# Optimization experiments

Hardware: AMD Instinct MI355X
Metric: run time of the kernel (lower is better)

The kernel has to match this reference:

```python
import jax, jax.numpy as jnp
import numpy as np

HEAD_SIZE = 64
INPUT_SIZE = 1024
B, T = 4, 4096


def setup_inputs() -> dict:
    key = jax.random.key(0)
    ks = jax.random.split(key, 7)
    s = 1.0 / np.sqrt(INPUT_SIZE)
    return {
        "x": jax.random.normal(ks[0], (B, T, INPUT_SIZE), dtype=jnp.float32),
        "Wk": jax.random.uniform(ks[1], (INPUT_SIZE, HEAD_SIZE), jnp.float32, -s, s),
        "bk": jax.random.uniform(ks[2], (HEAD_SIZE,), jnp.float32, -s, s),
        "Wq": jax.random.uniform(ks[3], (INPUT_SIZE, HEAD_SIZE), jnp.float32, -s, s),
        "bq": jax.random.uniform(ks[4], (HEAD_SIZE,), jnp.float32, -s, s),
        "Wv": jax.random.uniform(ks[5], (INPUT_SIZE, HEAD_SIZE), jnp.float32, -s, s),
        "bv": jax.random.uniform(ks[6], (HEAD_SIZE,), jnp.float32, -s, s),
    }


def reference(x, Wk, bk, Wq, bq, Wv, bv) -> jnp.ndarray:
    # x: [B, T, D]
    Tlen = x.shape[1]
    k = x @ Wk + bk          # [B, T, H]
    q = x @ Wq + bq          # [B, T, H]
    v = x @ Wv + bv          # [B, T, H]
    scale = 1.0 / jnp.sqrt(jnp.float32(HEAD_SIZE))
    # NOTE: original computes k @ q^T (not q @ k^T) -- keep that exact math.
    w = jnp.einsum("bth,bsh->bts", k, q) * scale  # [B, T, T]
    causal = jnp.tril(jnp.ones((Tlen, Tlen), dtype=bool))
    w = jnp.where(causal, w, -jnp.inf)
    w = jax.nn.softmax(w, axis=-1)
    out = jnp.einsum("bts,bsh->bth", w, v)        # [B, T, H]
    return out
```

## Files before the change

### kernel.cpp

```cpp
#include <hip/hip_runtime.h>
#include <hip/hip_bf16.h>
#include <stdint.h>

typedef __attribute__((ext_vector_type(8))) short short8;
typedef __attribute__((ext_vector_type(4))) float floatx4;

#define HD 64
#define D_IN 1024
#define TLEN 4096
#define NB 4
#define PPB 144
#define LDP 72
#define SL2E 0.18033688011112042f

__device__ __forceinline__ short f2bf(float f) {
    union { float f; uint32_t u; } v{f};
    uint32_t u = v.u;
    uint32_t r = (u + 0x7FFFu + ((u >> 16) & 1u)) >> 16;
    return (short)r;
}

__device__ __forceinline__ float bf2f(short s) {
    union { uint32_t u; float f; } v;
    v.u = ((uint32_t)(uint16_t)s) << 16;
    return v.f;
}

__device__ __forceinline__ uint32_t pk2(float a, float b) {
    __hip_bfloat162 h = __float22bfloat162_rn(float2{a, b});
    union { __hip_bfloat162 h; uint32_t u; } c{h};
    return c.u;
}

__device__ __forceinline__ void ld_lds16(const void* g, void* l) {
    __builtin_amdgcn_global_load_lds(
        (const __attribute__((address_space(1))) uint32_t*)g,
        (__attribute__((address_space(3))) uint32_t*)l, 16, 0, 0);
}

__global__ __launch_bounds__(256) void prep_w(const float* __restrict__ Wk,
                                              const float* __restrict__ Wq,
                                              const float* __restrict__ Wv,
                                              short* __restrict__ wt) {
    int i = blockIdx.x * 256 + threadIdx.x;
    int j  = i & 7;
    int l  = (i >> 3) & 63;
    int ks = (i >> 9) & 1;
    int rest = i >> 10;
    int f  = rest % 12;
    int kt = rest / 12;
    int mat = f >> 2, nt = f & 3;
    int n = nt * 16 + (l & 15);
    int k = kt * 64 + ks * 32 + (l >> 4) * 8 + j;
    const float* W = (mat == 0) ? Wk : ((mat == 1) ? Wq : Wv);
    wt[i] = f2bf(W[(size_t)k * 64 + n]);
}

__global__ __launch_bounds__(256) void proj(const float* __restrict__ x,
                                            const float* __restrict__ bk,
                                            const float* __restrict__ bq,
                                            const float* __restrict__ bv,
                                            const short* __restrict__ wt,
                                            short* __restrict__ ko,
                                            short* __restrict__ qo,
                                            short* __restrict__ vt) {
    __shared__ float xs[2][2048];
    __shared__ short ws2[2][12288];

    int tid = threadIdx.x;
    int wave = tid >> 6, lane = tid & 63;
    int quad = lane >> 4, l16 = lane & 15;
    int row0 = blockIdx.x * 32;
    int wbase = tid & ~63;

    floatx4 acc[2][3];
#pragma unroll
    for (int mt = 0; mt < 2; mt++)
#pragma unroll
        for (int fi = 0; fi < 3; fi++) acc[mt][fi] = (floatx4){0.f, 0.f, 0.f, 0.f};

    auto stage = [&](int kt, int buf) {
#pragma unroll
        for (int it = 0; it < 2; it++) {
            int s = it * 256 + tid;
            int r = s >> 4, p = s & 15;
            int c = (((p >> 1) ^ (r & 7)) << 1) | (p & 1);
            ld_lds16(x + (size_t)(row0 + r) * D_IN + kt * 64 + c * 4,
                     &xs[buf][(it * 256 + wbase) * 4]);
        }
#pragma unroll
        for (int it = 0; it < 6; it++) {
            int s = it * 256 + tid;
            ld_lds16(wt + (size_t)kt * 12288 + (size_t)s * 8,
                     &ws2[buf][(it * 256 + wbase) * 8]);
        }
    };

    stage(0, 0);
    for (int kt = 0; kt < 16; kt++) {
        int buf = kt & 1;
        __syncthreads();
        if (kt < 15) stage(kt + 1, buf ^ 1);
#pragma unroll
        for (int ks = 0; ks < 2; ks++) {
            short8 av[2];
#pragma unroll
            for (int mt = 0; mt < 2; mt++) {
                int r = mt * 16 + l16;
                int g = ks * 4 + quad;
                const float4* pp = reinterpret_cast<const float4*>(
                    &xs[buf][r * 64 + ((g ^ (r & 7)) << 1) * 4]);
                float4 f0 = pp[0], f1 = pp[1];
                union { uint32_t u[4]; short8 s; } cv;
                cv.u[0] = pk2(f0.x, f0.y); cv.u[1] = pk2(f0.z, f0.w);
                cv.u[2] = pk2(f1.x, f1.y); cv.u[3] = pk2(f1.z, f1.w);
                av[mt] = cv.s;
            }
#pragma unroll
            for (int fi = 0; fi < 3; fi++) {
                int f = wave * 3 + fi;
                short8 bf = *reinterpret_cast<const short8*>(
                    &ws2[buf][((f * 2 + ks) * 64 + lane) * 8]);
#pragma unroll
                for (int mt = 0; mt < 2; mt++)
                    acc[mt][fi] = __builtin_amdgcn_mfma_f32_16x16x32_bf16(av[mt], bf, acc[mt][fi], 0, 0, 0);
            }
        }
    }

#pragma unroll
    for (int fi = 0; fi < 3; fi++) {
        int f = wave * 3 + fi;
        int mat = f >> 2, nt = f & 3;
        int col = nt * 16 + l16;
        const float* bias = (mat == 0) ? bk : ((mat == 1) ? bq : bv);
        float bb = bias[col];
#pragma unroll
        for (int mt = 0; mt < 2; mt++)
#pragma unroll
            for (int reg = 0; reg < 4; reg++) {
                float v = acc[mt][fi][reg] + bb;
                int row = row0 + mt * 16 + quad * 4 + reg;
                if (mat == 0) ko[(size_t)row * HD + col] = f2bf(v * SL2E);
                else if (mat == 1) qo[(size_t)row * HD + col] = f2bf(v);
                else {
                    int bt = row >> 12, tl = row & 4095;
                    vt[(size_t)bt * HD * TLEN + (size_t)col * TLEN + tl] = f2bf(v);
                }
            }
    }
}

template<int SPLIT>
__global__ __launch_bounds__(256) void attn_kern(const short* __restrict__ kb,
                                                 const short* __restrict__ qb,
                                                 const short* __restrict__ vtw,
                                                 short* __restrict__ pO,
                                                 float* __restrict__ pL,
                                                 float* __restrict__ out) {
    __shared__ short Ks[2][4096];
    __shared__ short Vs[2][4096];
    __shared__ short Ps[128 * LDP];

    int tid = threadIdx.x;
    int wave = tid >> 6, lane = tid & 63;
    int quad = lane >> 4, l16 = lane & 15;
    int wbase = tid & ~63;
    int batch = blockIdx.y;

    int tile, j0, j1, slot = 0, nparts = 1;
    if (SPLIT) {
        int bx = blockIdx.x;
        int t = 0, accb = 0;
        for (;;) { int p = (2 * t + 9) >> 3; if (bx < accb + p) break; accb += p; ++t; }
        tile = t;
        j0 = (bx - accb) * 8;
        int je = j0 + 8, lim = 2 * tile + 2;
        j1 = je < lim ? je : lim;
        slot = batch * PPB + bx;
        nparts = (2 * tile + 9) >> 3;
    } else {
        tile = 31 - blockIdx.x;
        j0 = 0; j1 = 2 * tile + 2;
    }
    int t0 = tile * 128;
    int jd = 2 * tile;
    size_t base = (size_t)batch * TLEN * HD;
    const short* vbase = vtw + (size_t)batch * HD * TLEN;

    short8 kf[2][2];
#pragma unroll
    for (int mt = 0; mt < 2; mt++) {
        int trow = t0 + wave * 32 + mt * 16 + l16;
#pragma unroll
        for (int ks = 0; ks < 2; ks++)
            kf[mt][ks] = *reinterpret_cast<const short8*>(kb + base + (size_t)trow * HD + ks * 32 + quad * 8);
    }

    floatx4 o_acc[2][4];
#pragma unroll
    for (int mt = 0; mt < 2; mt++)
#pragma unroll
        for (int ht = 0; ht < 4; ht++) o_acc[mt][ht] = (floatx4){0.f, 0.f, 0.f, 0.f};
    float l_p[2] = {0.f, 0.f};

    auto stage = [&](int j, int buf) {
        int s0 = j * 64;
#pragma unroll
        for (int it = 0; it < 2; it++) {
            int s = it * 256 + tid;
            int r = s >> 3, c = (s & 7) ^ (r & 7);
            ld_lds16(qb + base + (size_t)(s0 + r) * HD + c * 8,
                     &Ks[buf][(it * 256 + wbase) * 8]);
            ld_lds16(vbase + (size_t)r * TLEN + s0 + c * 8,
                     &Vs[buf][(it * 256 + wbase) * 8]);
        }
    };

    stage(j0, 0);
    for (int j = j0; j < j1; ++j) {
        int buf = (j - j0) & 1;
        __syncthreads();
        if (j + 1 < j1) stage(j + 1, buf ^ 1);

        if (j == jd + 1 && wave < 2) continue;

        floatx4 sacc[2][4];
#pragma unroll
        for (int mt = 0; mt < 2; mt++)
#pragma unroll
            for (int nt = 0; nt < 4; nt++) sacc[mt][nt] = (floatx4){0.f, 0.f, 0.f, 0.f};
#pragma unroll
        for (int ks = 0; ks < 2; ks++)
#pragma unroll
            for (int nt = 0; nt < 4; nt++) {
                int r = nt * 16 + l16, g = ks * 4 + quad;
                short8 a = *reinterpret_cast<const short8*>(
                    &Ks[buf][r * 64 + (g ^ (r & 7)) * 8]);
#pragma unroll
                for (int mt = 0; mt < 2; mt++)
                    sacc[mt][nt] = __builtin_amdgcn_mfma_f32_16x16x32_bf16(a, kf[mt][ks], sacc[mt][nt], 0, 0, 0);
            }

        float pv[2][4][4];
#pragma unroll
        for (int mt = 0; mt < 2; mt++)
#pragma unroll
            for (int nt = 0; nt < 4; nt++)
#pragma unroll
                for (int reg = 0; reg < 4; reg++)
                    pv[mt][nt][reg] = __builtin_amdgcn_exp2f(sacc[mt][nt][reg]);
        if (j >= jd) {
            int s0 = j * 64;
#pragma unroll
            for (int mt = 0; mt < 2; mt++) {
                int t_g = t0 + wave * 32 + mt * 16 + l16;
#pragma unroll
                for (int nt = 0; nt < 4; nt++) {
                    int s_g = s0 + nt * 16 + quad * 4;
#pragma unroll
                    for (int reg = 0; reg < 4; reg++)
                        if (s_g + reg > t_g) pv[mt][nt][reg] = 0.f;
                }
            }
        }
#pragma unroll
        for (int mt = 0; mt < 2; mt++) {
            l_p[mt] += ((pv[mt][0][0] + pv[mt][0][1]) + (pv[mt][0][2] + pv[mt][0][3]))
                     + ((pv[mt][1][0] + pv[mt][1][1]) + (pv[mt][1][2] + pv[mt][1][3]))
                     + ((pv[mt][2][0] + pv[mt][2][1]) + (pv[mt][2][2] + pv[mt][2][3]))
                     + ((pv[mt][3][0] + pv[mt][3][1]) + (pv[mt][3][2] + pv[mt][3][3]));
#pragma unroll
            for (int nt = 0; nt < 4; nt++) {
                union { uint32_t u[2]; uint64_t q; } w;
                w.u[0] = pk2(pv[mt][nt][0], pv[mt][nt][1]);
                w.u[1] = pk2(pv[mt][nt][2], pv[mt][nt][3]);
                int row = wave * 32 + mt * 16 + l16;
                *reinterpret_cast<uint64_t*>(&Ps[row * LDP + nt * 16 + quad * 4]) = w.q;
            }
        }

#pragma unroll
        for (int ks = 0; ks < 2; ks++) {
            short8 a[2];
#pragma unroll
            for (int mt = 0; mt < 2; mt++)
                a[mt] = *reinterpret_cast<const short8*>(
                    &Ps[(wave * 32 + mt * 16 + l16) * LDP + ks * 32 + quad * 8]);
#pragma unroll
            for (int ht = 0; ht < 4; ht++) {
                int r = ht * 16 + l16, g = ks * 4 + quad;
                short8 b = *reinterpret_cast<const short8*>(
                    &Vs[buf][r * 64 + (g ^ (r & 7)) * 8]);
#pragma unroll
                for (int mt = 0; mt < 2; mt++)
                    o_acc[mt][ht] = __builtin_amdgcn_mfma_f32_16x16x32_bf16(a[mt], b, o_acc[mt][ht], 0, 0, 0);
            }
        }
    }

#pragma unroll
    for (int mt = 0; mt < 2; mt++) {
        l_p[mt] += __shfl_xor(l_p[mt], 16);
        l_p[mt] += __shfl_xor(l_p[mt], 32);
    }

    if (SPLIT && nparts > 1) {
        short* po = pO + (size_t)slot * 8192;
#pragma unroll
        for (int mt = 0; mt < 2; mt++)
#pragma unroll
            for (int ht = 0; ht < 4; ht++)
#pragma unroll
                for (int reg = 0; reg < 4; reg++) {
                    int lr = wave * 32 + mt * 16 + quad * 4 + reg;
                    po[lr * 64 + ht * 16 + l16] = f2bf(o_acc[mt][ht][reg]);
                }
        if (quad == 0) {
#pragma unroll
            for (int mt = 0; mt < 2; mt++)
                pL[(size_t)slot * 128 + wave * 32 + mt * 16 + l16] = l_p[mt];
        }
    } else {
#pragma unroll
        for (int mt = 0; mt < 2; mt++) {
#pragma unroll
            for (int reg = 0; reg < 4; reg++) {
                float L = __shfl(l_p[mt], quad * 4 + reg, 64);
                float inv = 1.0f / L;
                int t = t0 + wave * 32 + mt * 16 + quad * 4 + reg;
#pragma unroll
                for (int ht = 0; ht < 4; ht++)
                    out[base + (size_t)t * HD + ht * 16 + l16] = o_acc[mt][ht][reg] * inv;
            }
        }
    }
}

__global__ __launch_bounds__(256) void attn_combine(const short* __restrict__ pO,
                                                    const float* __restrict__ pL,
                                                    float* __restrict__ out) {
    int tile = blockIdx.x + 4, batch = blockIdx.y;
    int nparts = (2 * tile + 9) >> 3;
    int a = tile >> 2, r = tile & 3;
    int slot0 = batch * PPB + 2 * a * (a + 1) + r * (a + 1);
    int t = threadIdx.x;
    int off = t * 32;
    int row = off >> 6;
    int col0 = off & 63;

    float L = 0.f;
    float acc[32];
#pragma unroll
    for (int i = 0; i < 32; i++) acc[i] = 0.f;

    for (int p = 0; p < nparts; ++p) {
        int slot = slot0 + p;
        L += pL[(size_t)slot * 128 + row];
        const short* src = pO + (size_t)slot * 8192 + off;
#pragma unroll
        for (int c = 0; c < 4; c++) {
            short8 v = *reinterpret_cast<const short8*>(src + c * 8);
#pragma unroll
            for (int i = 0; i < 8; i++) acc[c * 8 + i] += bf2f(v[i]);
        }
    }
    float inv = 1.0f / L;
    float4* dstp = reinterpret_cast<float4*>(out + (size_t)batch * TLEN * HD +
                                             (size_t)(tile * 128 + row) * HD + col0);
#pragma unroll
    for (int c = 0; c < 8; c++) {
        float4 v;
        v.x = acc[c * 4 + 0] * inv; v.y = acc[c * 4 + 1] * inv;
        v.z = acc[c * 4 + 2] * inv; v.w = acc[c * 4 + 3] * inv;
        dstp[c] = v;
    }
}

extern "C" void kernel_launch(void* const* d_in, const int* in_sizes, int n_in,
                              void* d_out, int out_size, void* d_ws, size_t ws_size,
                              hipStream_t stream) {
    const float* x  = (const float*)d_in[0];
    const float* Wk = (const float*)d_in[1];
    const float* bk = (const float*)d_in[2];
    const float* Wq = (const float*)d_in[3];
    const float* bq = (const float*)d_in[4];
    const float* Wv = (const float*)d_in[5];
    const float* bv = (const float*)d_in[6];
    float* out = (float*)d_out;

    const size_t nrow = (size_t)NB * TLEN;
    short* ko = (short*)d_ws;
    short* qo = ko + nrow * HD;
    short* vt = qo + nrow * HD;
    short* wt = vt + nrow * HD;
    short* pO = wt + 3 * 64 * 1024;
    float* pL = (float*)(pO + (size_t)NB * PPB * 8192);
    size_t need = (size_t)((char*)(pL + (size_t)NB * PPB * 128) - (char*)d_ws);

    prep_w<<<768, 256, 0, stream>>>(Wk, Wq, Wv, wt);
    proj<<<512, 256, 0, stream>>>(x, bk, bq, bv, wt, ko, qo, vt);
    if (ws_size >= need) {
        attn_kern<1><<<dim3(PPB, NB), 256, 0, stream>>>(ko, qo, vt, pO, pL, out);
        attn_combine<<<dim3(28, NB), 256, 0, stream>>>(pO, pL, out);
    } else {
        attn_kern<0><<<dim3(32, NB), 256, 0, stream>>>(ko, qo, vt, nullptr, nullptr, out);
    }
}
```

Measured before the change: 152.5 us.

## Split-K projection with two wave groups and 64-row tiles reduced through LDS

```diff
diff --git a/kernel.cpp b/kernel.cpp
--- a/kernel.cpp
+++ b/kernel.cpp
@@ -12,6 +12,7 @@
 #define PPB 144
 #define LDP 72
 #define SL2E 0.18033688011112042f
+#define WSZ 196608
 
 __device__ __forceinline__ short f2bf(float f) {
     union { float f; uint32_t u; } v{f};
@@ -45,18 +46,17 @@
     int i = blockIdx.x * 256 + threadIdx.x;
     int j  = i & 7;
     int l  = (i >> 3) & 63;
-    int ks = (i >> 9) & 1;
-    int rest = i >> 10;
+    int rest = i >> 9;
     int f  = rest % 12;
-    int kt = rest / 12;
+    int ck = rest / 12;
     int mat = f >> 2, nt = f & 3;
     int n = nt * 16 + (l & 15);
-    int k = kt * 64 + ks * 32 + (l >> 4) * 8 + j;
+    int k = ck * 32 + (l >> 4) * 8 + j;
     const float* W = (mat == 0) ? Wk : ((mat == 1) ? Wq : Wv);
     wt[i] = f2bf(W[(size_t)k * 64 + n]);
 }
 
-__global__ __launch_bounds__(256) void proj(const float* __restrict__ x,
+__global__ __launch_bounds__(512) void proj(const float* __restrict__ x,
                                             const float* __restrict__ bk,
                                             const float* __restrict__ bq,
                                             const float* __restrict__ bv,
@@ -64,90 +64,104 @@
                                             short* __restrict__ ko,
                                             short* __restrict__ qo,
                                             short* __restrict__ vt) {
-    __shared__ float xs[2][2048];
-    __shared__ short ws2[2][12288];
+    __shared__ float xs[2][2][2048];
+    __shared__ short ws[2][2][6144];
+    __shared__ float red[12 * 1024];
 
     int tid = threadIdx.x;
     int wave = tid >> 6, lane = tid & 63;
+    int grp = wave >> 2, gw = wave & 3;
     int quad = lane >> 4, l16 = lane & 15;
-    int row0 = blockIdx.x * 32;
-    int wbase = tid & ~63;
-
-    floatx4 acc[2][3];
-#pragma unroll
-    for (int mt = 0; mt < 2; mt++)
+    int gtid = tid & 255;
+    int gwbase = gtid & ~63;
+    int row0 = blockIdx.x * 64;
+
+    floatx4 acc[4][3];
+#pragma unroll
+    for (int mt = 0; mt < 4; mt++)
 #pragma unroll
         for (int fi = 0; fi < 3; fi++) acc[mt][fi] = (floatx4){0.f, 0.f, 0.f, 0.f};
 
-    auto stage = [&](int kt, int buf) {
+    auto stage = [&](int ck, int buf) {
 #pragma unroll
         for (int it = 0; it < 2; it++) {
-            int s = it * 256 + tid;
-            int r = s >> 4, p = s & 15;
-            int c = (((p >> 1) ^ (r & 7)) << 1) | (p & 1);
-            ld_lds16(x + (size_t)(row0 + r) * D_IN + kt * 64 + c * 4,
-                     &xs[buf][(it * 256 + wbase) * 4]);
-        }
-#pragma unroll
-        for (int it = 0; it < 6; it++) {
-            int s = it * 256 + tid;
-            ld_lds16(wt + (size_t)kt * 12288 + (size_t)s * 8,
-                     &ws2[buf][(it * 256 + wbase) * 8]);
+            int s = it * 256 + gtid;
+            int r = s >> 3, c = s & 7;
+            int sc = ((((c >> 1) ^ (r & 3)) << 1) | (c & 1));
+            ld_lds16(x + (size_t)(row0 + r) * D_IN + ck * 32 + sc * 4,
+                     &xs[grp][buf][(it * 256 + gwbase) * 4]);
+        }
+#pragma unroll
+        for (int it = 0; it < 3; it++) {
+            int s = it * 256 + gtid;
+            ld_lds16(wt + (size_t)ck * 6144 + (size_t)s * 8,
+                     &ws[grp][buf][(it * 256 + gwbase) * 8]);
         }
     };
 
-    stage(0, 0);
-    for (int kt = 0; kt < 16; kt++) {
-        int buf = kt & 1;
+    int ck0 = grp * 16;
+    stage(ck0, 0);
+    for (int i = 0; i < 16; i++) {
+        int buf = i & 1;
         __syncthreads();
-        if (kt < 15) stage(kt + 1, buf ^ 1);
-#pragma unroll
-        for (int ks = 0; ks < 2; ks++) {
-            short8 av[2];
-#pragma unroll
-            for (int mt = 0; mt < 2; mt++) {
-                int r = mt * 16 + l16;
-                int g = ks * 4 + quad;
-                const float4* pp = reinterpret_cast<const float4*>(
-                    &xs[buf][r * 64 + ((g ^ (r & 7)) << 1) * 4]);
-                float4 f0 = pp[0], f1 = pp[1];
-                union { uint32_t u[4]; short8 s; } cv;
-                cv.u[0] = pk2(f0.x, f0.y); cv.u[1] = pk2(f0.z, f0.w);
-                cv.u[2] = pk2(f1.x, f1.y); cv.u[3] = pk2(f1.z, f1.w);
-                av[mt] = cv.s;
-            }
-#pragma unroll
-            for (int fi = 0; fi < 3; fi++) {
-                int f = wave * 3 + fi;
-                short8 bf = *reinterpret_cast<const short8*>(
-                    &ws2[buf][((f * 2 + ks) * 64 + lane) * 8]);
-#pragma unroll
-                for (int mt = 0; mt < 2; mt++)
-                    acc[mt][fi] = __builtin_amdgcn_mfma_f32_16x16x32_bf16(av[mt], bf, acc[mt][fi], 0, 0, 0);
-            }
-        }
-    }
-
-#pragma unroll
-    for (int fi = 0; fi < 3; fi++) {
-        int f = wave * 3 + fi;
-        int mat = f >> 2, nt = f & 3;
-        int col = nt * 16 + l16;
-        const float* bias = (mat == 0) ? bk : ((mat == 1) ? bq : bv);
-        float bb = bias[col];
-#pragma unroll
-        for (int mt = 0; mt < 2; mt++)
-#pragma unroll
-            for (int reg = 0; reg < 4; reg++) {
-                float v = acc[mt][fi][reg] + bb;
-                int row = row0 + mt * 16 + quad * 4 + reg;
-                if (mat == 0) ko[(size_t)row * HD + col] = f2bf(v * SL2E);
-                else if (mat == 1) qo[(size_t)row * HD + col] = f2bf(v);
-                else {
-                    int bt = row >> 12, tl = row & 4095;
-                    vt[(size_t)bt * HD * TLEN + (size_t)col * TLEN + tl] = f2bf(v);
+        if (i < 15) stage(ck0 + i + 1, buf ^ 1);
+
+        short8 av[4];
+#pragma unroll
+        for (int mt = 0; mt < 4; mt++) {
+            int r = mt * 16 + l16;
+            const float4* pp = reinterpret_cast<const float4*>(
+                &xs[grp][buf][r * 32 + ((quad ^ (r & 3)) << 1) * 4]);
+            float4 f0 = pp[0], f1 = pp[1];
+            union { uint32_t u[4]; short8 s; } cv;
+            cv.u[0] = pk2(f0.x, f0.y); cv.u[1] = pk2(f0.z, f0.w);
+            cv.u[2] = pk2(f1.x, f1.y); cv.u[3] = pk2(f1.z, f1.w);
+            av[mt] = cv.s;
+        }
+#pragma unroll
+        for (int fi = 0; fi < 3; fi++) {
+            int f = gw * 3 + fi;
+            short8 bf = *reinterpret_cast<const short8*>(
+                &ws[grp][buf][(f * 64 + lane) * 8]);
+#pragma unroll
+            for (int mt = 0; mt < 4; mt++)
+                acc[mt][fi] = __builtin_amdgcn_mfma_f32_16x16x32_bf16(av[mt], bf, acc[mt][fi], 0, 0, 0);
+        }
+    }
+
+    __syncthreads();
+    if (grp == 1) {
+#pragma unroll
+        for (int mt = 0; mt < 4; mt++)
+#pragma unroll
+            for (int fi = 0; fi < 3; fi++)
+                *reinterpret_cast<floatx4*>(&red[(mt * 3 + fi) * 1024 + gtid * 4]) = acc[mt][fi];
+    }
+    __syncthreads();
+    if (grp == 0) {
+#pragma unroll
+        for (int fi = 0; fi < 3; fi++) {
+            int f = gw * 3 + fi;
+            int mat = f >> 2, nt = f & 3;
+            int col = nt * 16 + l16;
+            const float* bias = (mat == 0) ? bk : ((mat == 1) ? bq : bv);
+            float bb = bias[col];
+#pragma unroll
+            for (int mt = 0; mt < 4; mt++) {
+                floatx4 o = *reinterpret_cast<const floatx4*>(&red[(mt * 3 + fi) * 1024 + gtid * 4]);
+#pragma unroll
+                for (int reg = 0; reg < 4; reg++) {
+                    float v = acc[mt][fi][reg] + o[reg] + bb;
+                    int row = row0 + mt * 16 + quad * 4 + reg;
+                    if (mat == 0) ko[(size_t)row * HD + col] = f2bf(v * SL2E);
+                    else if (mat == 1) qo[(size_t)row * HD + col] = f2bf(v);
+                    else {
+                        int bt = row >> 12, tl = row & 4095;
+                        vt[(size_t)bt * HD * TLEN + (size_t)col * TLEN + tl] = f2bf(v);
+                    }
                 }
             }
+        }
     }
 }
 
@@ -394,12 +408,12 @@
     short* qo = ko + nrow * HD;
     short* vt = qo + nrow * HD;
     short* wt = vt + nrow * HD;
-    short* pO = wt + 3 * 64 * 1024;
+    short* pO = wt + WSZ;
     float* pL = (float*)(pO + (size_t)NB * PPB * 8192);
     size_t need = (size_t)((char*)(pL + (size_t)NB * PPB * 128) - (char*)d_ws);
 
     prep_w<<<768, 256, 0, stream>>>(Wk, Wq, Wv, wt);
-    proj<<<512, 256, 0, stream>>>(x, bk, bq, bv, wt, ko, qo, vt);
+    proj<<<256, 512, 0, stream>>>(x, bk, bq, bv, wt, ko, qo, vt);
     if (ws_size >= need) {
         attn_kern<1><<<dim3(PPB, NB), 256, 0, stream>>>(ko, qo, vt, pO, pL, out);
         attn_combine<<<dim3(28, NB), 256, 0, stream>>>(pO, pL, out);
```

After: 155.9 us. 2.2% more time.

## Load projection weights directly into registers and split combine across more blocks

Applied to the files above, without the earlier changes.

```diff
diff --git a/kernel.cpp b/kernel.cpp
--- a/kernel.cpp
+++ b/kernel.cpp
@@ -12,6 +12,7 @@
 #define PPB 144
 #define LDP 72
 #define SL2E 0.18033688011112042f
+#define WSZ 196608
 
 __device__ __forceinline__ short f2bf(float f) {
     union { float f; uint32_t u; } v{f};
@@ -65,7 +66,6 @@
                                             short* __restrict__ qo,
                                             short* __restrict__ vt) {
     __shared__ float xs[2][2048];
-    __shared__ short ws2[2][12288];
 
     int tid = threadIdx.x;
     int wave = tid >> 6, lane = tid & 63;
@@ -79,7 +79,7 @@
 #pragma unroll
         for (int fi = 0; fi < 3; fi++) acc[mt][fi] = (floatx4){0.f, 0.f, 0.f, 0.f};
 
-    auto stage = [&](int kt, int buf) {
+    auto stagex = [&](int kt, int buf) {
 #pragma unroll
         for (int it = 0; it < 2; it++) {
             int s = it * 256 + tid;
@@ -88,19 +88,24 @@
             ld_lds16(x + (size_t)(row0 + r) * D_IN + kt * 64 + c * 4,
                      &xs[buf][(it * 256 + wbase) * 4]);
         }
-#pragma unroll
-        for (int it = 0; it < 6; it++) {
-            int s = it * 256 + tid;
-            ld_lds16(wt + (size_t)kt * 12288 + (size_t)s * 8,
-                     &ws2[buf][(it * 256 + wbase) * 8]);
-        }
     };
 
-    stage(0, 0);
-    for (int kt = 0; kt < 16; kt++) {
+    const short* wv0 = wt + (size_t)(((wave * 3) * 2) * 64 + lane) * 8;
+
+    auto wload = [&](int kt, short8 (&wf)[3][2]) {
+#pragma unroll
+        for (int fi = 0; fi < 3; fi++)
+#pragma unroll
+            for (int ks = 0; ks < 2; ks++)
+                wf[fi][ks] = *reinterpret_cast<const short8*>(
+                    wv0 + (size_t)kt * 12288 + (size_t)((fi * 2 + ks) * 64) * 8);
+    };
+
+    auto body = [&](int kt, short8 (&wcur)[3][2], short8 (&wnxt)[3][2]) {
         int buf = kt & 1;
+        if (kt < 15) stagex(kt + 1, buf ^ 1);
         __syncthreads();
-        if (kt < 15) stage(kt + 1, buf ^ 1);
+        if (kt < 15) wload(kt + 1, wnxt);
 #pragma unroll
         for (int ks = 0; ks < 2; ks++) {
             short8 av[2];
@@ -118,14 +123,20 @@
             }
 #pragma unroll
             for (int fi = 0; fi < 3; fi++) {
-                int f = wave * 3 + fi;
-                short8 bf = *reinterpret_cast<const short8*>(
-                    &ws2[buf][((f * 2 + ks) * 64 + lane) * 8]);
 #pragma unroll
                 for (int mt = 0; mt < 2; mt++)
-                    acc[mt][fi] = __builtin_amdgcn_mfma_f32_16x16x32_bf16(av[mt], bf, acc[mt][fi], 0, 0, 0);
-            }
-        }
+                    acc[mt][fi] = __builtin_amdgcn_mfma_f32_16x16x32_bf16(av[mt], wcur[fi][ks], acc[mt][fi], 0, 0, 0);
+            }
+        }
+        __syncthreads();
+    };
+
+    short8 wA[3][2], wB[3][2];
+    wload(0, wA);
+    stagex(0, 0);
+    for (int kt = 0; kt < 16; kt += 2) {
+        body(kt, wA, wB);
+        body(kt + 1, wB, wA);
     }
 
 #pragma unroll
@@ -340,36 +351,32 @@
 __global__ __launch_bounds__(256) void attn_combine(const short* __restrict__ pO,
                                                     const float* __restrict__ pL,
                                                     float* __restrict__ out) {
-    int tile = blockIdx.x + 4, batch = blockIdx.y;
+    int tile = blockIdx.x + 4, batch = blockIdx.y, rq = blockIdx.z;
     int nparts = (2 * tile + 9) >> 3;
     int a = tile >> 2, r = tile & 3;
     int slot0 = batch * PPB + 2 * a * (a + 1) + r * (a + 1);
     int t = threadIdx.x;
-    int off = t * 32;
+    int off = rq * 2048 + t * 8;
     int row = off >> 6;
     int col0 = off & 63;
 
     float L = 0.f;
-    float acc[32];
-#pragma unroll
-    for (int i = 0; i < 32; i++) acc[i] = 0.f;
+    float acc[8];
+#pragma unroll
+    for (int i = 0; i < 8; i++) acc[i] = 0.f;
 
     for (int p = 0; p < nparts; ++p) {
         int slot = slot0 + p;
         L += pL[(size_t)slot * 128 + row];
-        const short* src = pO + (size_t)slot * 8192 + off;
-#pragma unroll
-        for (int c = 0; c < 4; c++) {
-            short8 v = *reinterpret_cast<const short8*>(src + c * 8);
-#pragma unroll
-            for (int i = 0; i < 8; i++) acc[c * 8 + i] += bf2f(v[i]);
-        }
+        short8 v = *reinterpret_cast<const short8*>(pO + (size_t)slot * 8192 + off);
+#pragma unroll
+        for (int i = 0; i < 8; i++) acc[i] += bf2f(v[i]);
     }
     float inv = 1.0f / L;
     float4* dstp = reinterpret_cast<float4*>(out + (size_t)batch * TLEN * HD +
                                              (size_t)(tile * 128 + row) * HD + col0);
 #pragma unroll
-    for (int c = 0; c < 8; c++) {
+    for (int c = 0; c < 2; c++) {
         float4 v;
         v.x = acc[c * 4 + 0] * inv; v.y = acc[c * 4 + 1] * inv;
         v.z = acc[c * 4 + 2] * inv; v.w = acc[c * 4 + 3] * inv;
@@ -394,7 +401,7 @@
     short* qo = ko + nrow * HD;
     short* vt = qo + nrow * HD;
     short* wt = vt + nrow * HD;
-    short* pO = wt + 3 * 64 * 1024;
+    short* pO = wt + WSZ;
     float* pL = (float*)(pO + (size_t)NB * PPB * 8192);
     size_t need = (size_t)((char*)(pL + (size_t)NB * PPB * 128) - (char*)d_ws);
 
@@ -402,7 +409,7 @@
     proj<<<512, 256, 0, stream>>>(x, bk, bq, bv, wt, ko, qo, vt);
     if (ws_size >= need) {
         attn_kern<1><<<dim3(PPB, NB), 256, 0, stream>>>(ko, qo, vt, pO, pL, out);
-        attn_combine<<<dim3(28, NB), 256, 0, stream>>>(pO, pL, out);
+        attn_combine<<<dim3(28, NB, 4), 256, 0, stream>>>(pO, pL, out);
     } else {
         attn_kern<0><<<dim3(32, NB), 256, 0, stream>>>(ko, qo, vt, nullptr, nullptr, out);
     }
```

Measured after the change: 149.6 us. About the same (-1.9%).
